# Kernel tuning notes

Hardware: AMD Instinct MI355X
Metric: run time of the kernel (lower is better)

## Reference

```python
import jax, jax.numpy as jnp
import numpy as np

TEMP = 30.0  # softmax temperature from init kwarg
NUM_EXPERTS = 4


def setup_inputs() -> dict:
    key = jax.random.key(0)
    ks = jax.random.split(key, 4)
    B, Cin, H, W = 32, 128, 56, 56
    Cout, K, E, R = 256, 3, NUM_EXPERTS, 16  # R = max(Cin//reduction, reduction)
    x = jax.random.normal(ks[0], (B, Cin, H, W), dtype=jnp.float32)
    # expert conv bank: torch.rand -> uniform[0,1)
    convs = jax.random.uniform(ks[1], (E, Cout, Cin, K, K), dtype=jnp.float32)
    # router MLP (nn.Linear has bias by default)
    w1 = jax.random.normal(ks[2], (R, Cin), dtype=jnp.float32) * 0.05
    b1 = jnp.zeros((R,), dtype=jnp.float32)
    w2 = jax.random.normal(ks[3], (E, R), dtype=jnp.float32) * 0.05
    b2 = jnp.zeros((E,), dtype=jnp.float32)
    return {"x": x, "convs": convs, "w1": w1, "b1": b1, "w2": w2, "b2": b2}


def reference(x, convs, w1, b1, w2, b2):
    B, Cin, H, W = x.shape
    E, Cout, _, K, _ = convs.shape
    # per-sample global average pool -> router MLP -> softmax(logits / temp)
    gap = x.mean(axis=(2, 3))                      # [B, Cin]
    h = jax.nn.relu(gap @ w1.T + b1)               # [B, R]
    logits = h @ w2.T + b2                         # [B, E]
    routing = jax.nn.softmax(logits / TEMP, axis=-1)
    # per-sample mixed conv kernels [B, Cout, Cin, K, K]
    kern = jnp.einsum('be,eoikl->boikl', routing, convs)
    # batched per-sample conv via grouped conv: treat batch as groups
    xg = x.reshape(1, B * Cin, H, W)
    kg = kern.reshape(B * Cout, Cin, K, K)
    out = jax.lax.conv_general_dilated(
        xg, kg,
        window_strides=(1, 1),
        padding=[(1, 1), (1, 1)],
        feature_group_count=B,
        dimension_numbers=('NCHW', 'OIHW', 'NCHW'))
    return out.reshape(B, Cout, out.shape[2], out.shape[3])
```

## Files before the change

kernel.cpp:

```cpp
#include <hip/hip_runtime.h>
#include <hip/hip_bf16.h>

#define NB   32
#define CIN  128
#define HH   56
#define WW   56
#define COUT 256
#define HW   3136
#define NCHUNK 576

typedef __bf16 bf16x8 __attribute__((ext_vector_type(8)));
typedef float floatx4 __attribute__((ext_vector_type(4)));

__global__ void xpose_wswz(const float* __restrict__ x, __hip_bfloat16* __restrict__ xT,
                           float* __restrict__ gpart,
                           const float* __restrict__ convs, __hip_bfloat16* __restrict__ convT) {
    __shared__ __align__(16) char smem[19008];
    int blk = blockIdx.x;
    if (blk < 3136) {
        int q = blk & 7, j = blk >> 3;
        int bl = j / 98, rj = j - bl * 98;
        int b = q * 4 + bl;
        int ih = rj / 49, hwb = rj - ih * 49;
        int hw0 = hwb * 64, i0 = ih * 64;
        float (*tile)[65] = (float(*)[65])smem;
        float (*red)[4]   = (float(*)[4])(smem + 16640);
        const float* xp = x + ((size_t)b * CIN + i0) * HW + hw0;
        for (int t = threadIdx.x; t < 1024; t += 256) {
            int ir = t >> 4, c4 = t & 15;
            float4 v = *(const float4*)(xp + (size_t)ir * HW + c4 * 4);
            tile[ir][c4 * 4 + 0] = v.x; tile[ir][c4 * 4 + 1] = v.y;
            tile[ir][c4 * 4 + 2] = v.z; tile[ir][c4 * 4 + 3] = v.w;
        }
        __syncthreads();
        __hip_bfloat16* op = xT + ((size_t)b * HW + hw0) * CIN + i0;
        for (int t = threadIdx.x; t < 512; t += 256) {
            int pp = t >> 3, seg = t & 7;
            __hip_bfloat16 tmp[8];
            #pragma unroll
            for (int jj = 0; jj < 8; ++jj) tmp[jj] = __float2bfloat16(tile[seg * 8 + jj][pp]);
            *(uint4*)(op + (size_t)pp * CIN + seg * 8) = *(uint4*)tmp;
        }
        int ch = threadIdx.x & 63, grp = threadIdx.x >> 6;
        float s = 0.f;
        #pragma unroll
        for (int k = 0; k < 16; ++k) s += tile[ch][grp * 16 + k];
        red[ch][grp] = s;
        __syncthreads();
        if (threadIdx.x < 64) {
            float t4 = red[threadIdx.x][0] + red[threadIdx.x][1]
                     + red[threadIdx.x][2] + red[threadIdx.x][3];
            gpart[((size_t)b * 49 + hwb) * CIN + i0 + threadIdx.x] = t4;
        }
    } else {
        int b2 = blk - 3136;
        int ks = b2 & 1, cc = (b2 >> 1) & 1, mt = (b2 >> 2) & 3;
        int wm = (b2 >> 4) & 1, mtile = (b2 >> 5) & 1, e = b2 >> 6;
        float (*tl)[297] = (float(*)[297])smem;
        int row0 = mtile * 128 + wm * 64 + mt * 16;
        const float* src = convs + (size_t)(e * COUT + row0) * 1152 + (cc * 64 + ks * 32) * 9;
        for (int i = threadIdx.x; i < 1152; i += 256) {
            int r = i / 72, o = i - r * 72;
            float4 v = *(const float4*)(src + (size_t)r * 1152 + o * 4);
            tl[r][o * 4 + 0] = v.x; tl[r][o * 4 + 1] = v.y;
            tl[r][o * 4 + 2] = v.z; tl[r][o * 4 + 3] = v.w;
        }
        __syncthreads();
        for (int i = threadIdx.x; i < 576; i += 256) {
            int p = i >> 6, lane = i & 63;
            int col = lane & 15, quad = lane >> 4;
            int c = mtile * 288 + p * 32 + cc * 16 + ks * 8 + mt * 2 + wm;
            __hip_bfloat16 tmp[8];
            #pragma unroll
            for (int jj = 0; jj < 8; ++jj)
                tmp[jj] = __float2bfloat16(tl[col][(quad * 8 + jj) * 9 + p]);
            *(uint4*)(convT + ((size_t)(e * NCHUNK + c) * 64 + lane) * 8) = *(uint4*)tmp;
        }
    }
}

__global__ void router_kernel(const float* __restrict__ gpart,
                              const float* __restrict__ w1, const float* __restrict__ b1,
                              const float* __restrict__ w2, const float* __restrict__ b2,
                              float* __restrict__ routing) {
    int blk = blockIdx.x;
    int b = (blk & 7) * 4 + (blk >> 3);
    int ch = threadIdx.x;
    __shared__ float gs[CIN];
    __shared__ float hs[16];
    float s = 0.f;
    #pragma unroll 7
    for (int hwb = 0; hwb < 49; ++hwb)
        s += gpart[((size_t)b * 49 + hwb) * CIN + ch];
    gs[ch] = s * (1.0f / HW);
    __syncthreads();
    if (ch < 16) {
        float a = 0.f;
        #pragma unroll
        for (int i = 0; i < CIN; ++i) a += gs[i] * w1[ch * CIN + i];
        hs[ch] = fmaxf(a + b1[ch], 0.f);
    }
    __syncthreads();
    if (ch == 0) {
        float lg[4], mx = -1e30f;
        #pragma unroll
        for (int e = 0; e < 4; ++e) {
            float a = b2[e];
            #pragma unroll
            for (int r = 0; r < 16; ++r) a += hs[r] * w2[e * 16 + r];
            lg[e] = a * (1.0f / 30.0f);
            mx = fmaxf(mx, lg[e]);
        }
        float den = 0.f, ex[4];
        #pragma unroll
        for (int e = 0; e < 4; ++e) { ex[e] = expf(lg[e] - mx); den += ex[e]; }
        #pragma unroll
        for (int e = 0; e < 4; ++e) routing[b * 4 + e] = ex[e] / den;
    }
}

__global__ void mix_kernel(const __hip_bfloat16* __restrict__ convT,
                           const float* __restrict__ routing,
                           __hip_bfloat16* __restrict__ wmix) {
    int blk = blockIdx.x, tid = threadIdx.x;
    int q = blk & 7, j = blk >> 3;
    int bl = j / 72;
    int b = q * 4 + bl;
    int jj = j - bl * 72;
    int pair = jj * 256 + tid;
    float r0 = routing[b * 4 + 0], r1 = routing[b * 4 + 1];
    float r2 = routing[b * 4 + 2], r3 = routing[b * 4 + 3];
    const size_t ES = (size_t)NCHUNK * 64 * 8;
    const __hip_bfloat16* sp = convT + (size_t)pair * 16;
    __hip_bfloat16 o[16];
    #pragma unroll
    for (int h = 0; h < 2; ++h) {
        bf16x8 w0 = *(const bf16x8*)(sp + h * 8);
        bf16x8 w1v = *(const bf16x8*)(sp + h * 8 + ES);
        bf16x8 w2v = *(const bf16x8*)(sp + h * 8 + 2 * ES);
        bf16x8 w3v = *(const bf16x8*)(sp + h * 8 + 3 * ES);
        #pragma unroll
        for (int k = 0; k < 8; ++k) {
            float v = r0 * (float)w0[k] + r1 * (float)w1v[k]
                    + r2 * (float)w2v[k] + r3 * (float)w3v[k];
            o[h * 8 + k] = __float2bfloat16(v);
        }
    }
    uint4* d = (uint4*)(wmix + ((size_t)b * 18432 + pair) * 16);
    d[0] = ((uint4*)o)[0];
    d[1] = ((uint4*)o)[1];
}

#define XSTRIDE 136
__global__ __launch_bounds__(256, 2)
void conv_mfma(const __hip_bfloat16* __restrict__ xT,
               const __hip_bfloat16* __restrict__ wmix,
               float* __restrict__ out) {
    __shared__ __align__(16) __hip_bfloat16 xs[180 * XSTRIDE];

    int lin = blockIdx.x;
    int wg  = (lin & 7) * 224 + (lin >> 3);
    int b   = wg / 56;
    int rr  = wg - b * 56;
    int mtile = rr / 28;
    int tile  = rr - mtile * 28;

    const int yt = tile >> 2, xt = tile & 3;
    const int y0 = yt * 8, x0 = xt * 16;
    const int tid = threadIdx.x;
    const int lane = tid & 63, wave = tid >> 6;
    const int wm = wave >> 1;
    const int mh = wave & 1;
    const int col = lane & 15, quad = lane >> 4;

    const __hip_bfloat16* xb = xT + (size_t)b * HW * CIN;
    const __hip_bfloat16* wptr = wmix +
        ((size_t)(b * NCHUNK + mtile * 288 + wm)) * 512 + lane * 8;

    #pragma unroll
    for (int j = 0; j < 12; ++j) {
        int tt = tid + j * 256;
        if (tt < 2880) {
            int pix = tt >> 4, seg = tt & 15;
            int py = pix / 18, px = pix - py * 18;
            int gy = y0 - 1 + py, gx = x0 - 1 + px;
            uint4 v = {0u, 0u, 0u, 0u};
            if ((unsigned)gy < 56u && (unsigned)gx < 56u)
                v = *(const uint4*)(xb + ((size_t)(gy * 56 + gx) * CIN + seg * 8));
            *(uint4*)(&xs[pix * XSTRIDE + seg * 8]) = v;
        }
    }

    floatx4 acc[2][8];
    #pragma unroll
    for (int mtl = 0; mtl < 2; ++mtl)
        #pragma unroll
        for (int nt = 0; nt < 8; ++nt)
            acc[mtl][nt] = (floatx4){0.f, 0.f, 0.f, 0.f};

    bf16x8 af[4][2];
    bf16x8 bfr[2][10];

    auto lda = [&](int u, bf16x8* dst) {
        const int g = u / 3, ky = u - g * 3;
        const int cc = g / 6, r6 = g - cc * 6;
        const int ks = r6 / 3, kx = r6 - ks * 3;
        const int pp = ky * 3 + kx;
        #pragma unroll
        for (int mtl = 0; mtl < 2; ++mtl)
            dst[mtl] = *(const bf16x8*)(wptr +
                (size_t)(pp * 32 + cc * 16 + ks * 8 + (mh * 2 + mtl) * 2) * 512);
    };
    auto ldb = [&](int g, bf16x8* dst) {
        const int cc = g / 6, r6 = g - cc * 6;
        const int ks = r6 / 3, kx = r6 - ks * 3;
        const int base = cc * 64 + ks * 32 + quad * 8;
        #pragma unroll
        for (int r = 0; r < 10; ++r)
            dst[r] = *(const bf16x8*)(&xs[(r * 18 + col + kx) * XSTRIDE + base]);
    };

    lda(0, af[0]); lda(1, af[1]); lda(2, af[2]);
    __syncthreads();
    ldb(0, bfr[0]);

    #pragma unroll
    for (int g = 0; g < 12; ++g) {
        if (g + 1 < 12) ldb(g + 1, bfr[(g + 1) & 1]);
        #pragma unroll
        for (int ky = 0; ky < 3; ++ky) {
            const int u = g * 3 + ky;
            if (u + 3 < 36) lda(u + 3, af[(u + 3) & 3]);
            __builtin_amdgcn_s_setprio(1);
            #pragma unroll
            for (int mtl = 0; mtl < 2; ++mtl)
                #pragma unroll
                for (int nt = 0; nt < 8; ++nt)
                    acc[mtl][nt] = __builtin_amdgcn_mfma_f32_16x16x32_bf16(
                        af[u & 3][mtl], bfr[g & 1][nt + ky], acc[mtl][nt], 0, 0, 0);
            __builtin_amdgcn_s_setprio(0);
        }
    }

    const int x = x0 + col;
    if (x < 56) {
        #pragma unroll
        for (int mtl = 0; mtl < 2; ++mtl) {
            int o = mtile * 128 + wave * 32 + mtl * 16 + quad * 4;
            #pragma unroll
            for (int nt = 0; nt < 8; ++nt) {
                int y = y0 + nt;
                float* op = out + (((size_t)b * COUT + o) * 56 + y) * 56 + x;
                #pragma unroll
                for (int r = 0; r < 4; ++r)
                    op[(size_t)r * HW] = acc[mtl][nt][r];
            }
        }
    }
}

extern "C" void kernel_launch(void* const* d_in, const int* in_sizes, int n_in,
                              void* d_out, int out_size, void* d_ws, size_t ws_size,
                              hipStream_t stream) {
    const float* x     = (const float*)d_in[0];
    const float* convs = (const float*)d_in[1];
    const float* w1    = (const float*)d_in[2];
    const float* b1    = (const float*)d_in[3];
    const float* w2    = (const float*)d_in[4];
    const float* b2    = (const float*)d_in[5];
    float* out = (float*)d_out;

    char* ws = (char*)d_ws;
    float* routing       = (float*)(ws + 16384);
    __hip_bfloat16* xT   = (__hip_bfloat16*)(ws + 16896);
    __hip_bfloat16* wmix = (__hip_bfloat16*)(ws + 16896 + 25690112);
    __hip_bfloat16* convT= (__hip_bfloat16*)(ws + 16896 + 25690112 + 18874368);
    float* gpart = (float*)wmix;

    xpose_wswz   <<<3392, 256, 0, stream>>>(x, xT, gpart, convs, convT);
    router_kernel<<<32, 128, 0, stream>>>(gpart, w1, b1, w2, b2, routing);
    mix_kernel   <<<2304, 256, 0, stream>>>(convT, routing, wmix);
    conv_mfma    <<<1792, 256, 0, stream>>>(xT, wmix, out);
}
```

Before: 210.4 us.

## Restructure conv MFMA operand prefetch per group and split router reduction across threads

In the conv kernel, the A-fragment prefetch now loads all three ky rows for the next group at once into a double buffer. The B fragments are no longer double-buffered and are loaded from LDS for the current group just before its MFMAs. This lowers register pressure on the B side and cuts the number of prefetch points, but it exposes LDS latency at the start of each group. The router kernel now uses 256 threads, with two halves each summing alternate partial-GAP rows, which shortens its serial reduction.

```diff
diff --git a/kernel.cpp b/kernel.cpp
--- a/kernel.cpp
+++ b/kernel.cpp
@@ -85,23 +85,27 @@
                               float* __restrict__ routing) {
     int blk = blockIdx.x;
     int b = (blk & 7) * 4 + (blk >> 3);
-    int ch = threadIdx.x;
+    int tid = threadIdx.x;
+    int ch = tid & 127, half = tid >> 7;
+    __shared__ float g2[2][CIN];
     __shared__ float gs[CIN];
     __shared__ float hs[16];
     float s = 0.f;
-    #pragma unroll 7
-    for (int hwb = 0; hwb < 49; ++hwb)
+    #pragma unroll 5
+    for (int hwb = half; hwb < 49; hwb += 2)
         s += gpart[((size_t)b * 49 + hwb) * CIN + ch];
-    gs[ch] = s * (1.0f / HW);
-    __syncthreads();
-    if (ch < 16) {
+    g2[half][ch] = s;
+    __syncthreads();
+    if (tid < CIN) gs[tid] = (g2[0][tid] + g2[1][tid]) * (1.0f / HW);
+    __syncthreads();
+    if (tid < 16) {
         float a = 0.f;
         #pragma unroll
-        for (int i = 0; i < CIN; ++i) a += gs[i] * w1[ch * CIN + i];
-        hs[ch] = fmaxf(a + b1[ch], 0.f);
-    }
-    __syncthreads();
-    if (ch == 0) {
+        for (int i = 0; i < CIN; ++i) a += gs[i] * w1[tid * CIN + i];
+        hs[tid] = fmaxf(a + b1[tid], 0.f);
+    }
+    __syncthreads();
+    if (tid == 0) {
         float lg[4], mx = -1e30f;
         #pragma unroll
         for (int e = 0; e < 4; ++e) {
@@ -198,48 +202,45 @@
         for (int nt = 0; nt < 8; ++nt)
             acc[mtl][nt] = (floatx4){0.f, 0.f, 0.f, 0.f};
 
-    bf16x8 af[4][2];
-    bf16x8 bfr[2][10];
-
-    auto lda = [&](int u, bf16x8* dst) {
-        const int g = u / 3, ky = u - g * 3;
-        const int cc = g / 6, r6 = g - cc * 6;
-        const int ks = r6 / 3, kx = r6 - ks * 3;
-        const int pp = ky * 3 + kx;
-        #pragma unroll
-        for (int mtl = 0; mtl < 2; ++mtl)
-            dst[mtl] = *(const bf16x8*)(wptr +
-                (size_t)(pp * 32 + cc * 16 + ks * 8 + (mh * 2 + mtl) * 2) * 512);
+    bf16x8 afb[2][6];
+    bf16x8 bfr[10];
+
+    auto ldaG = [&](int g, bf16x8* dst) {
+        const int cc = g / 6, r6g = g - cc * 6;
+        const int ks = r6g / 3, kx = r6g - ks * 3;
+        #pragma unroll
+        for (int ky = 0; ky < 3; ++ky)
+            #pragma unroll
+            for (int mtl = 0; mtl < 2; ++mtl)
+                dst[ky * 2 + mtl] = *(const bf16x8*)(wptr +
+                    (size_t)((ky * 3 + kx) * 32 + cc * 16 + ks * 8 + (mh * 2 + mtl) * 2) * 512);
     };
-    auto ldb = [&](int g, bf16x8* dst) {
-        const int cc = g / 6, r6 = g - cc * 6;
-        const int ks = r6 / 3, kx = r6 - ks * 3;
+    auto ldbG = [&](int g, bf16x8* dst) {
+        const int cc = g / 6, r6g = g - cc * 6;
+        const int ks = r6g / 3, kx = r6g - ks * 3;
         const int base = cc * 64 + ks * 32 + quad * 8;
         #pragma unroll
         for (int r = 0; r < 10; ++r)
             dst[r] = *(const bf16x8*)(&xs[(r * 18 + col + kx) * XSTRIDE + base]);
     };
 
-    lda(0, af[0]); lda(1, af[1]); lda(2, af[2]);
-    __syncthreads();
-    ldb(0, bfr[0]);
+    ldaG(0, afb[0]);
+    __syncthreads();
 
     #pragma unroll
     for (int g = 0; g < 12; ++g) {
-        if (g + 1 < 12) ldb(g + 1, bfr[(g + 1) & 1]);
-        #pragma unroll
-        for (int ky = 0; ky < 3; ++ky) {
-            const int u = g * 3 + ky;
-            if (u + 3 < 36) lda(u + 3, af[(u + 3) & 3]);
-            __builtin_amdgcn_s_setprio(1);
+        if (g + 1 < 12) ldaG(g + 1, afb[(g + 1) & 1]);
+        ldbG(g, bfr);
+        __builtin_amdgcn_s_setprio(1);
+        #pragma unroll
+        for (int ky = 0; ky < 3; ++ky)
             #pragma unroll
             for (int mtl = 0; mtl < 2; ++mtl)
                 #pragma unroll
                 for (int nt = 0; nt < 8; ++nt)
                     acc[mtl][nt] = __builtin_amdgcn_mfma_f32_16x16x32_bf16(
-                        af[u & 3][mtl], bfr[g & 1][nt + ky], acc[mtl][nt], 0, 0, 0);
-            __builtin_amdgcn_s_setprio(0);
-        }
+                        afb[g & 1][ky * 2 + mtl], bfr[nt + ky], acc[mtl][nt], 0, 0, 0);
+        __builtin_amdgcn_s_setprio(0);
     }
 
     const int x = x0 + col;
@@ -278,7 +279,7 @@
     float* gpart = (float*)wmix;
 
     xpose_wswz   <<<3392, 256, 0, stream>>>(x, xT, gpart, convs, convT);
-    router_kernel<<<32, 128, 0, stream>>>(gpart, w1, b1, w2, b2, routing);
+    router_kernel<<<32, 256, 0, stream>>>(gpart, w1, b1, w2, b2, routing);
     mix_kernel   <<<2304, 256, 0, stream>>>(convT, routing, wmix);
     conv_mfma    <<<1792, 256, 0, stream>>>(xT, wmix, out);
 }
```

After: 210.6 us. About the same (+0.1%).
